# Kernel tuning notes

Measured on AMD Instinct MI355X. Metric: run time of the kernel, lower is better.

## Reference

```python
import jax, jax.numpy as jnp
import numpy as np

HIDDEN = 4096
NQ = 32        # query heads
NKV = 8        # kv heads
HD = 128       # head dim
EPS = 1e-6
BASE = 10000.0
T = 2048


def setup_inputs() -> dict:
    key = jax.random.key(0)
    ks = jax.random.split(key, 4)
    s = 0.02
    return {
        "hidden_states": jax.random.normal(ks[0], (T, HIDDEN), jnp.float32),
        "w_qkv": jax.random.normal(ks[1], ((NQ + 2 * NKV) * HD, HIDDEN), jnp.float32) * s,
        "q_norm_w": jnp.ones((HD,), jnp.float32),
        "k_norm_w": jnp.ones((HD,), jnp.float32),
        "w_o": jax.random.normal(ks[2], (HIDDEN, NQ * HD), jnp.float32) * s,
        "positions": jnp.arange(T, dtype=jnp.int64),
    }


def _rms_norm(x, w):
    # x: [T, H, D], normalize over last dim
    var = jnp.mean(jnp.square(x), axis=-1, keepdims=True)
    return x * jax.lax.rsqrt(var + EPS) * w


def _rope(x, positions):
    # neox-style: split halves. x: [T, H, D]
    half = HD // 2
    inv_freq = 1.0 / (BASE ** (jnp.arange(0, HD, 2, dtype=jnp.float32) / HD))  # [half]
    ang = positions.astype(jnp.float32)[:, None] * inv_freq  # [T, half]
    cos = jnp.cos(ang)[:, None, :]  # [T, 1, half]
    sin = jnp.sin(ang)[:, None, :]
    x1, x2 = x[..., :half], x[..., half:]
    return jnp.concatenate([x1 * cos - x2 * sin, x2 * cos + x1 * sin], axis=-1)


def reference(hidden_states, w_qkv, q_norm_w, k_norm_w, w_o, positions):
    t = hidden_states.shape[0]
    qkv = hidden_states @ w_qkv.T  # [T, (NQ+2*NKV)*HD]
    q, k, v = jnp.split(qkv, [NQ * HD, (NQ + NKV) * HD], axis=-1)
    q = _rms_norm(q.reshape(t, NQ, HD), q_norm_w)
    k = _rms_norm(k.reshape(t, NKV, HD), k_norm_w)
    v = v.reshape(t, NKV, HD)
    q = _rope(q, positions)
    k = _rope(k, positions)

    g = NQ // NKV
    qg = q.reshape(t, NKV, g, HD).transpose(1, 2, 0, 3)  # [NKV, g, T, HD]
    kt = k.transpose(1, 0, 2)  # [NKV, T, HD]
    vt = v.transpose(1, 0, 2)
    scale = HD ** -0.5
    scores = jnp.einsum('hgqd,hkd->hgqk', qg, kt) * scale  # [NKV, g, T, T]
    causal = positions[:, None] >= positions[None, :]  # [T, T]
    scores = jnp.where(causal[None, None], scores, jnp.float32(-1e30))
    p = jax.nn.softmax(scores, axis=-1)
    o = jnp.einsum('hgqk,hkd->hgqd', p, vt)  # [NKV, g, T, HD]
    o = o.transpose(2, 0, 1, 3).reshape(t, NQ * HD)
    return o @ w_o.T
```

## Files before the change

### kernel.cpp

```cpp
#include <hip/hip_runtime.h>
#include <hip/hip_bf16.h>

typedef float f32x4 __attribute__((ext_vector_type(4)));
typedef short s16x8 __attribute__((ext_vector_type(8)));
typedef short s16x4 __attribute__((ext_vector_type(4)));
typedef unsigned short u16;

#define HIDDEN 4096
#define NQ 32
#define NKV 8
#define HD 128
#define T_SEQ 2048
#define QKV_N ((NQ + 2 * NKV) * HD)

__device__ __forceinline__ u16 f2bf(float f) {
    union { float f; unsigned u; } v; v.f = f;
    unsigned r = v.u + 0x7FFFu + ((v.u >> 16) & 1u);
    return (u16)(r >> 16);
}
__device__ __forceinline__ float b2f(u16 h) {
    union { unsigned u; float f; } v; v.u = ((unsigned)h) << 16; return v.f;
}
__device__ __forceinline__ void gload_lds16(const u16* g, u16* l) {
    __builtin_amdgcn_global_load_lds(
        (const __attribute__((address_space(1))) unsigned int*)g,
        (__attribute__((address_space(3))) unsigned int*)l,
        16, 0, 0);
}
__device__ __forceinline__ int xcd_swz(int flat, int nwg) {
    return (flat & 7) * (nwg >> 3) + (flat >> 3);
}

__device__ __forceinline__ void conv8(const float* src, u16* dst, int i) {
    const float4 a = ((const float4*)src)[2 * i];
    const float4 b = ((const float4*)src)[2 * i + 1];
    s16x8 o;
    o[0] = (short)f2bf(a.x); o[1] = (short)f2bf(a.y);
    o[2] = (short)f2bf(a.z); o[3] = (short)f2bf(a.w);
    o[4] = (short)f2bf(b.x); o[5] = (short)f2bf(b.y);
    o[6] = (short)f2bf(b.z); o[7] = (short)f2bf(b.w);
    ((s16x8*)dst)[i] = o;
}
__global__ __launch_bounds__(256) void conv2_bf16_kern(
    const float* __restrict__ s1, u16* __restrict__ d1, int n1,
    const float* __restrict__ s2, u16* __restrict__ d2, int n2)
{
    for (int i = blockIdx.x * 256 + threadIdx.x; i < n1 + n2; i += gridDim.x * 256) {
        if (i < n1) conv8(s1, d1, i);
        else        conv8(s2, d2, i - n1);
    }
}

__global__ __launch_bounds__(512) void gemm1_4ph(
    const u16* __restrict__ A, const u16* __restrict__ B,
    u16* __restrict__ C, int N, int K)
{
    __shared__ u16 As[2][256 * 64];
    __shared__ u16 Bs[2][192 * 64];
    const int tid = threadIdx.x, lane = tid & 63, wid = tid >> 6;
    const int wr = wid >> 2, wc = wid & 3;
    const int lg = lane >> 4, l15 = lane & 15;
    const int m0 = blockIdx.y * 256, n0 = blockIdx.x * 192;
    const int nk = K >> 6;
    const int r8 = lane >> 3;
    const int csw = ((lane & 7) ^ r8) * 8;

    f32x4 acc[8][3] = {};
    s16x8 af[4][2], bq[3][2];

    auto stageA = [&](int sl, int c, int kt) {
        gload_lds16(&A[(size_t)(m0 + c * 64 + wid * 8 + r8) * K + kt * 64 + csw],
                    &As[sl][(c * 64 + wid * 8) * 64]);
    };
    auto stageB = [&](int sl, int c, int kt) {
        gload_lds16(&B[(size_t)(n0 + c * 64 + wid * 8 + r8) * K + kt * 64 + csw],
                    &Bs[sl][(c * 64 + wid * 8) * 64]);
    };
    auto ldA2 = [&](int s_, int mh_) {
#pragma unroll
        for (int mi = 0; mi < 4; ++mi)
#pragma unroll
            for (int kh = 0; kh < 2; ++kh)
                af[mi][kh] = *(const s16x8*)&As[s_][
                    ((wr * 128 + mh_ * 64 + mi * 16 + l15) << 6) +
                    (((lg + kh * 4) ^ (l15 & 7)) << 3)];
    };
    auto ldB2 = [&](int s_) {
#pragma unroll
        for (int ni = 0; ni < 3; ++ni)
#pragma unroll
            for (int kh = 0; kh < 2; ++kh)
                bq[ni][kh] = *(const s16x8*)&Bs[s_][
                    ((wc * 48 + ni * 16 + l15) << 6) +
                    (((lg + kh * 4) ^ (l15 & 7)) << 3)];
    };
    auto mm2 = [&](int mh_) {
        __builtin_amdgcn_s_setprio(1);
#pragma unroll
        for (int mi = 0; mi < 4; ++mi)
#pragma unroll
            for (int ni = 0; ni < 3; ++ni)
#pragma unroll
                for (int kh = 0; kh < 2; ++kh)
                    acc[mh_ * 4 + mi][ni] =
                        __builtin_amdgcn_mfma_f32_16x16x32_bf16(
                            af[mi][kh], bq[ni][kh], acc[mh_ * 4 + mi][ni], 0, 0, 0);
        __builtin_amdgcn_s_setprio(0);
    };
#define FENCE asm volatile("" ::: "memory");

    stageA(0, 0, 0); stageA(0, 1, 0); stageA(0, 2, 0); stageA(0, 3, 0);
    stageB(0, 0, 0); stageB(0, 1, 0); stageB(0, 2, 0);
    stageA(1, 0, 1); stageA(1, 2, 1);
    asm volatile("s_waitcnt vmcnt(2)" ::: "memory");
    __builtin_amdgcn_s_barrier();

    for (int t = 0; t < nk; ++t) {
        const int s = t & 1;
        ldA2(s, 0); ldB2(s);
        if (t + 1 < nk) {
            stageA(s ^ 1, 1, t + 1); stageA(s ^ 1, 3, t + 1);
            stageB(s ^ 1, 0, t + 1); stageB(s ^ 1, 1, t + 1); stageB(s ^ 1, 2, t + 1);
        }
        FENCE
        __builtin_amdgcn_s_barrier();
        mm2(0);
        FENCE
        __builtin_amdgcn_s_barrier();
        ldA2(s, 1);
        if (t + 2 < nk) { stageA(s, 0, t + 2); stageA(s, 2, t + 2); }
        FENCE
        __builtin_amdgcn_s_barrier();
        mm2(1);
        if (t + 2 < nk) asm volatile("s_waitcnt vmcnt(2)" ::: "memory");
        else            asm volatile("s_waitcnt vmcnt(0)" ::: "memory");
        FENCE
        __builtin_amdgcn_s_barrier();
    }

#pragma unroll
    for (int mh = 0; mh < 2; ++mh)
#pragma unroll
    for (int mi = 0; mi < 4; ++mi)
#pragma unroll
    for (int ni = 0; ni < 3; ++ni) {
        int row0 = m0 + wr * 128 + mh * 64 + mi * 16 + lg * 4;
        int col  = n0 + wc * 48 + ni * 16 + l15;
#pragma unroll
        for (int r = 0; r < 4; ++r)
            C[(size_t)(row0 + r) * N + col] = f2bf(acc[mh * 4 + mi][ni][r]);
    }
}

__global__ __launch_bounds__(512) void gemm2_2ph(
    const u16* __restrict__ A, const u16* __restrict__ B,
    float* __restrict__ C, int N, int K)
{
    __shared__ u16 As[3][256 * 64];
    __shared__ u16 Bs[3][128 * 64];
    const int tid = threadIdx.x, lane = tid & 63, wid = tid >> 6;
    const int wr = wid >> 2, wc = wid & 3;
    const int lg = lane >> 4, l15 = lane & 15;
    const int m0 = blockIdx.y * 256, n0 = blockIdx.x * 128;
    const int nk = K >> 6;
    const int r8 = lane >> 3;
    const int csw = ((lane & 7) ^ r8) * 8;

    f32x4 acc[8][2] = {};
    s16x8 af[8][2], bq[2][2];

    auto stageAll = [&](int sl, int kt) {
#pragma unroll
        for (int c = 0; c < 4; ++c)
            gload_lds16(&A[(size_t)(m0 + c * 64 + wid * 8 + r8) * K + kt * 64 + csw],
                        &As[sl][(c * 64 + wid * 8) * 64]);
#pragma unroll
        for (int c = 0; c < 2; ++c)
            gload_lds16(&B[(size_t)(n0 + c * 64 + wid * 8 + r8) * K + kt * 64 + csw],
                        &Bs[sl][(c * 64 + wid * 8) * 64]);
    };
    auto ldAll = [&](int s_) {
#pragma unroll
        for (int mi = 0; mi < 8; ++mi)
#pragma unroll
            for (int kh = 0; kh < 2; ++kh)
                af[mi][kh] = *(const s16x8*)&As[s_][
                    ((wr * 128 + mi * 16 + l15) << 6) +
                    (((lg + kh * 4) ^ (l15 & 7)) << 3)];
#pragma unroll
        for (int ni = 0; ni < 2; ++ni)
#pragma unroll
            for (int kh = 0; kh < 2; ++kh)
                bq[ni][kh] = *(const s16x8*)&Bs[s_][
                    ((wc * 32 + ni * 16 + l15) << 6) +
                    (((lg + kh * 4) ^ (l15 & 7)) << 3)];
    };
    auto mmAll = [&]() {
        __builtin_amdgcn_s_setprio(1);
#pragma unroll
        for (int mi = 0; mi < 8; ++mi)
#pragma unroll
            for (int ni = 0; ni < 2; ++ni)
#pragma unroll
                for (int kh = 0; kh < 2; ++kh)
                    acc[mi][ni] = __builtin_amdgcn_mfma_f32_16x16x32_bf16(
                        af[mi][kh], bq[ni][kh], acc[mi][ni], 0, 0, 0);
        __builtin_amdgcn_s_setprio(0);
    };
#define FENCE asm volatile("" ::: "memory");

    stageAll(0, 0);
    stageAll(1, 1);
    asm volatile("s_waitcnt vmcnt(6)" ::: "memory");
    __builtin_amdgcn_s_barrier();

    int s = 0;
    for (int t = 0; t < nk; ++t) {
        ldAll(s);
        if (t + 2 < nk) {
            int s2 = s + 2; if (s2 >= 3) s2 -= 3;
            stageAll(s2, t + 2);
        }
        FENCE
        __builtin_amdgcn_s_barrier();
        mmAll();
        if (t + 2 < nk) asm volatile("s_waitcnt vmcnt(6)" ::: "memory");
        else            asm volatile("s_waitcnt vmcnt(0)" ::: "memory");
        FENCE
        __builtin_amdgcn_s_barrier();
        if (++s >= 3) s -= 3;
    }
#undef FENCE

#pragma unroll
    for (int mi = 0; mi < 8; ++mi)
#pragma unroll
    for (int ni = 0; ni < 2; ++ni) {
        int row0 = m0 + wr * 128 + mi * 16 + lg * 4;
        int col  = n0 + wc * 32 + ni * 16 + l15;
#pragma unroll
        for (int r = 0; r < 4; ++r)
            C[(size_t)(row0 + r) * N + col] = acc[mi][ni][r];
    }
}

__global__ __launch_bounds__(256) void nr_vt_kern(
    const u16* __restrict__ qkv, const float* __restrict__ qw,
    const float* __restrict__ kw, u16* __restrict__ qr, u16* __restrict__ kr,
    u16* __restrict__ vt)
{
    __shared__ u16 Ts[128][66];
    const int id = blockIdx.x, tid = threadIdx.x;
    if (id < 20480) {
        const int t = id & 2047, h = (id >> 11) * 4 + (tid >> 6);
        const int i = tid & 63;
        const size_t rowbase = (size_t)t * QKV_N;
        const u16* src; const float* w; u16* dst;
        if (h < 32) {
            src = qkv + rowbase + h * HD; w = qw;
            dst = qr + ((size_t)h * T_SEQ + t) * HD;
        } else {
            int kh = h - 32;
            src = qkv + rowbase + NQ * HD + kh * HD; w = kw;
            dst = kr + ((size_t)kh * T_SEQ + t) * HD;
        }
        float x1 = b2f(src[i]), x2 = b2f(src[i + 64]);
        float ss = x1 * x1 + x2 * x2;
#pragma unroll
        for (int d = 32; d >= 1; d >>= 1) ss += __shfl_xor(ss, d);
        float rs = rsqrtf(ss * (1.0f / 128.0f) + 1e-6f);
        x1 *= rs * w[i];
        x2 *= rs * w[i + 64];
        float ang = (float)t * exp2f((float)i * -0.20762050593567985f);
        float sn, cs;
        sincosf(ang, &sn, &cs);
        dst[i]      = f2bf(x1 * cs - x2 * sn);
        dst[i + 64] = f2bf(x2 * cs + x1 * sn);
        return;
    }
    const int id2 = id - 20480;
    const int t0 = (id2 & 31) * 64, kh = id2 >> 5;
#pragma unroll
    for (int it = 0; it < 4; ++it) {
        int slot = tid + it * 256;
        int tl = slot >> 4, dc = (slot & 15) * 8;
        s16x8 v = *(const s16x8*)&qkv[(size_t)(t0 + tl) * QKV_N + (NQ + NKV) * HD + kh * HD + dc];
#pragma unroll
        for (int e = 0; e < 8; ++e) Ts[dc + e][tl] = (u16)v[e];
    }
    __syncthreads();
#pragma unroll
    for (int it = 0; it < 4; ++it) {
        int slot = tid + it * 256;
        int d = slot >> 3, c = (slot & 7) * 8;
        s16x8 v = *(const s16x8*)&Ts[d][c];
        *(s16x8*)&vt[((size_t)kh * HD + d) * T_SEQ + t0 + c] = v;
    }
}

#define KS(b, r, c) Ks[(b)][((r) << 7) + ((c) ^ (((r) & 7) << 3))]
#define VS(b, r, c) Vs[(b)][((r) << 6) + ((c) ^ (((r) & 7) << 3))]
#define PS(wv, r, c) Ps[((wv) << 10) + ((r) << 6) + ((c) ^ (((r) & 7) << 3))]

__global__ __launch_bounds__(512) void attn_kern(
    const u16* __restrict__ qr, const u16* __restrict__ kr,
    const u16* __restrict__ vt, u16* __restrict__ o,
    const float* __restrict__ wo, u16* __restrict__ wo_bf)
{
    __shared__ u16 Ks[2][64 * 128];
    __shared__ u16 Vs[2][128 * 64];
    __shared__ u16 Ps[8 * 16 * 64];
    const int tid = threadIdx.x, lane = tid & 63, w = tid >> 6;
    const int lg = lane >> 4, l15 = lane & 15;
    const int fb = (int)blockIdx.y * 8 + (int)blockIdx.x;
    const int flat = xcd_swz(fb, 256);
    const int qh = flat >> 3, bx = flat & 7;
    const int kvh = qh >> 2;
    const float scale2 = 0.08838834764831845f * 1.4426950408889634f;

    const int cvbase = fb * 8192 + tid;
    int cv = 0;
    float4 cva = {}, cvb = {};

    const int krow = tid >> 4, kcol = (tid & 15) * 8;
    const int vrow = tid >> 3, vcol = (tid & 7) * 8;
    const u16* krbase = kr + (size_t)kvh * T_SEQ * HD;
    const u16* vtbase = vt + (size_t)kvh * HD * T_SEQ;

    s16x8 kst[2], vst[2];
#define LOADKV(k0_) do { \
    kst[0] = *(const s16x8*)&krbase[(size_t)((k0_) + krow) * HD + kcol]; \
    kst[1] = *(const s16x8*)&krbase[(size_t)((k0_) + krow + 32) * HD + kcol]; \
    vst[0] = *(const s16x8*)&vtbase[(size_t)(vrow) * T_SEQ + (k0_) + vcol]; \
    vst[1] = *(const s16x8*)&vtbase[(size_t)(vrow + 64) * T_SEQ + (k0_) + vcol]; \
    } while (0)
#define WRITEKV(b) do { \
    *(s16x8*)&KS((b), krow, kcol) = kst[0]; \
    *(s16x8*)&KS((b), krow + 32, kcol) = kst[1]; \
    *(s16x8*)&VS((b), vrow, vcol) = vst[0]; \
    *(s16x8*)&VS((b), vrow + 64, vcol) = vst[1]; \
    } while (0)

    for (int half = 0; half < 2; ++half) {
        const int q0 = (half == 0) ? bx * 128 : (T_SEQ - 128) - bx * 128;
        s16x8 qf[4];
        {
            const u16* qb = qr + ((size_t)qh * T_SEQ + q0 + w * 16 + l15) * HD;
#pragma unroll
            for (int dc = 0; dc < 4; ++dc) qf[dc] = *(const s16x8*)&qb[dc * 32 + lg * 8];
        }
        f32x4 oacc[8] = {};
        float mQ = -1e30f, lsQ = 0.f;

        const int ktiles = (q0 >> 6) + 2;
        LOADKV(0);
        WRITEKV(0);
        __syncthreads();
        for (int kt = 0; kt < ktiles; ++kt) {
            const int k0 = kt * 64;
            const int cur = kt & 1;
            if (kt + 1 < ktiles) LOADKV(k0 + 64);

            if (cv <= 16) {
                if (cv > 0) {
                    s16x8 o8;
                    o8[0] = (short)f2bf(cva.x); o8[1] = (short)f2bf(cva.y);
                    o8[2] = (short)f2bf(cva.z); o8[3] = (short)f2bf(cva.w);
                    o8[4] = (short)f2bf(cvb.x); o8[5] = (short)f2bf(cvb.y);
                    o8[6] = (short)f2bf(cvb.z); o8[7] = (short)f2bf(cvb.w);
                    ((s16x8*)wo_bf)[cvbase + (cv - 1) * 512] = o8;
                }
                if (cv < 16) {
                    cva = ((const float4*)wo)[2 * (cvbase + cv * 512)];
                    cvb = ((const float4*)wo)[2 * (cvbase + cv * 512) + 1];
                }
                ++cv;
            }

            f32x4 sc[4] = {};
            __builtin_amdgcn_s_setprio(1);
#pragma unroll
            for (int nc = 0; nc < 4; ++nc)
#pragma unroll
                for (int dc = 0; dc < 4; ++dc) {
                    s16x8 kf = *(const s16x8*)&KS(cur, nc * 16 + l15, dc * 32 + lg * 8);
                    sc[nc] = __builtin_amdgcn_mfma_f32_16x16x32_bf16(kf, qf[dc], sc[nc], 0, 0, 0);
                }
            __builtin_amdgcn_s_setprio(0);

            const int qg = q0 + w * 16 + l15;
            const bool needMask = (k0 + 63) > (q0 + w * 16);
            float tm = -1e30f;
#pragma unroll
            for (int nc = 0; nc < 4; ++nc)
#pragma unroll
                for (int r = 0; r < 4; ++r) {
                    float v = sc[nc][r] * scale2;
                    int kg = k0 + nc * 16 + lg * 4 + r;
                    if (needMask && kg > qg) v = -1e30f;
                    sc[nc][r] = v;
                    tm = fmaxf(tm, v);
                }
            tm = fmaxf(tm, __shfl_xor(tm, 16));
            tm = fmaxf(tm, __shfl_xor(tm, 32));

            if (__any(tm > mQ + 8.0f)) {
                float mn = fmaxf(mQ, tm);
                float alpha = exp2f(mQ - mn);
                mQ = mn;
                lsQ *= alpha;
                float aq[4];
#pragma unroll
                for (int r = 0; r < 4; ++r) aq[r] = __shfl(alpha, lg * 4 + r);
#pragma unroll
                for (int dc = 0; dc < 8; ++dc)
#pragma unroll
                    for (int r = 0; r < 4; ++r) oacc[dc][r] *= aq[r];
            }

            float ts = 0.f;
#pragma unroll
            for (int nc = 0; nc < 4; ++nc) {
                s16x4 pk;
#pragma unroll
                for (int r = 0; r < 4; ++r) {
                    float e = exp2f(sc[nc][r] - mQ);
                    ts += e;
                    pk[r] = (short)f2bf(e);
                }
                *(s16x4*)&PS(w, l15, nc * 16 + lg * 4) = pk;
            }
            ts += __shfl_xor(ts, 16);
            ts += __shfl_xor(ts, 32);
            lsQ += ts;

            __builtin_amdgcn_s_setprio(1);
#pragma unroll
            for (int kc = 0; kc < 2; ++kc) {
                s16x8 pf = *(const s16x8*)&PS(w, l15, kc * 32 + lg * 8);
#pragma unroll
                for (int dc = 0; dc < 8; ++dc) {
                    s16x8 vf = *(const s16x8*)&VS(cur, dc * 16 + l15, kc * 32 + lg * 8);
                    oacc[dc] = __builtin_amdgcn_mfma_f32_16x16x32_bf16(pf, vf, oacc[dc], 0, 0, 0);
                }
            }
            __builtin_amdgcn_s_setprio(0);

            if (kt + 1 < ktiles) WRITEKV(cur ^ 1);
            __syncthreads();
        }
        float lq[4];
#pragma unroll
        for (int r = 0; r < 4; ++r) lq[r] = __shfl(lsQ, lg * 4 + r);
#pragma unroll
        for (int r = 0; r < 4; ++r) {
            float inv = 1.0f / lq[r];
            int trow = q0 + w * 16 + lg * 4 + r;
            u16* dst = o + (size_t)trow * (NQ * HD) + qh * HD;
#pragma unroll
            for (int dc = 0; dc < 8; ++dc) dst[dc * 16 + l15] = f2bf(oacc[dc][r] * inv);
        }
    }
#undef LOADKV
#undef WRITEKV
}

extern "C" void kernel_launch(void* const* d_in, const int* in_sizes, int n_in,
                              void* d_out, int out_size, void* d_ws, size_t ws_size,
                              hipStream_t stream)
{
    const float* hs   = (const float*)d_in[0];
    const float* wqkv = (const float*)d_in[1];
    const float* qw   = (const float*)d_in[2];
    const float* kw   = (const float*)d_in[3];
    const float* wo   = (const float*)d_in[4];
    float* out = (float*)d_out;

    char* ws = (char*)d_ws;
    u16* hs_bf   = (u16*)(ws);
    u16* ob      = (u16*)(ws);
    u16* qkv_bf  = (u16*)(ws + 16777216);
    u16* wo_bf   = (u16*)(ws + 16777216);
    u16* wqkv_bf = (u16*)(ws + 41943040);
    u16* qr      = (u16*)(ws + 67108864);
    u16* kr      = (u16*)(ws + 83886080);
    u16* vt      = (u16*)(ws + 88080384);

    conv2_bf16_kern<<<2048, 256, 0, stream>>>(
        hs, hs_bf, T_SEQ * HIDDEN / 8, wqkv, wqkv_bf, QKV_N * HIDDEN / 8);
    gemm1_4ph<<<dim3(QKV_N / 192, T_SEQ / 256), 512, 0, stream>>>(
        hs_bf, wqkv_bf, qkv_bf, QKV_N, HIDDEN);
    nr_vt_kern<<<20736, 256, 0, stream>>>(qkv_bf, qw, kw, qr, kr, vt);
    attn_kern<<<dim3(8, NQ), 512, 0, stream>>>(qr, kr, vt, ob, wo, wo_bf);
    gemm2_2ph<<<dim3(HIDDEN / 128, T_SEQ / 256), 512, 0, stream>>>(
        ob, wo_bf, out, HIDDEN, HIDDEN);
}
```

Measured before the change: 301.5 us.

## Restructure QKV GEMM to two-phase loop with triple-buffered A tiles

Replaces the four-phase per-k-step schedule of the QKV projection GEMM with a two-phase one. All A and B fragments are loaded from LDS at once, then all MFMAs run. A tiles get a third LDS buffer so the next-next A tile can be prefetched while B is double-buffered. The aim is to halve barriers per k-step and give longer uninterrupted MFMA runs. The cost is more registers (8x2 A fragments held at once) and more LDS (an extra 32KB buffer), which could lower occupancy or cause spills.

Result: no change. 299.4 us (-0.7%).

```diff
diff --git a/kernel.cpp b/kernel.cpp
--- a/kernel.cpp
+++ b/kernel.cpp
@@ -51,11 +51,11 @@
     }
 }
 
-__global__ __launch_bounds__(512) void gemm1_4ph(
+__global__ __launch_bounds__(512) void gemm1_2ph(
     const u16* __restrict__ A, const u16* __restrict__ B,
     u16* __restrict__ C, int N, int K)
 {
-    __shared__ u16 As[2][256 * 64];
+    __shared__ u16 As[3][256 * 64];
     __shared__ u16 Bs[2][192 * 64];
     const int tid = threadIdx.x, lane = tid & 63, wid = tid >> 6;
     const int wr = wid >> 2, wc = wid & 3;
@@ -66,89 +66,85 @@
     const int csw = ((lane & 7) ^ r8) * 8;
 
     f32x4 acc[8][3] = {};
-    s16x8 af[4][2], bq[3][2];
-
-    auto stageA = [&](int sl, int c, int kt) {
-        gload_lds16(&A[(size_t)(m0 + c * 64 + wid * 8 + r8) * K + kt * 64 + csw],
-                    &As[sl][(c * 64 + wid * 8) * 64]);
-    };
-    auto stageB = [&](int sl, int c, int kt) {
-        gload_lds16(&B[(size_t)(n0 + c * 64 + wid * 8 + r8) * K + kt * 64 + csw],
-                    &Bs[sl][(c * 64 + wid * 8) * 64]);
-    };
-    auto ldA2 = [&](int s_, int mh_) {
-#pragma unroll
-        for (int mi = 0; mi < 4; ++mi)
+    s16x8 af[8][2], bq[3][2];
+
+    auto stageA = [&](int sl, int kt) {
+#pragma unroll
+        for (int c = 0; c < 4; ++c)
+            gload_lds16(&A[(size_t)(m0 + c * 64 + wid * 8 + r8) * K + kt * 64 + csw],
+                        &As[sl][(c * 64 + wid * 8) * 64]);
+    };
+    auto stageB = [&](int sl, int kt) {
+#pragma unroll
+        for (int c = 0; c < 3; ++c)
+            gload_lds16(&B[(size_t)(n0 + c * 64 + wid * 8 + r8) * K + kt * 64 + csw],
+                        &Bs[sl][(c * 64 + wid * 8) * 64]);
+    };
+    auto ldAll = [&](int s3_, int s2_) {
+#pragma unroll
+        for (int mi = 0; mi < 8; ++mi)
 #pragma unroll
             for (int kh = 0; kh < 2; ++kh)
-                af[mi][kh] = *(const s16x8*)&As[s_][
-                    ((wr * 128 + mh_ * 64 + mi * 16 + l15) << 6) +
+                af[mi][kh] = *(const s16x8*)&As[s3_][
+                    ((wr * 128 + mi * 16 + l15) << 6) +
                     (((lg + kh * 4) ^ (l15 & 7)) << 3)];
-    };
-    auto ldB2 = [&](int s_) {
 #pragma unroll
         for (int ni = 0; ni < 3; ++ni)
 #pragma unroll
             for (int kh = 0; kh < 2; ++kh)
-                bq[ni][kh] = *(const s16x8*)&Bs[s_][
+                bq[ni][kh] = *(const s16x8*)&Bs[s2_][
                     ((wc * 48 + ni * 16 + l15) << 6) +
                     (((lg + kh * 4) ^ (l15 & 7)) << 3)];
     };
-    auto mm2 = [&](int mh_) {
+    auto mmAll = [&]() {
         __builtin_amdgcn_s_setprio(1);
 #pragma unroll
-        for (int mi = 0; mi < 4; ++mi)
+        for (int mi = 0; mi < 8; ++mi)
 #pragma unroll
             for (int ni = 0; ni < 3; ++ni)
 #pragma unroll
                 for (int kh = 0; kh < 2; ++kh)
-                    acc[mh_ * 4 + mi][ni] =
-                        __builtin_amdgcn_mfma_f32_16x16x32_bf16(
-                            af[mi][kh], bq[ni][kh], acc[mh_ * 4 + mi][ni], 0, 0, 0);
+                    acc[mi][ni] = __builtin_amdgcn_mfma_f32_16x16x32_bf16(
+                        af[mi][kh], bq[ni][kh], acc[mi][ni], 0, 0, 0);
         __builtin_amdgcn_s_setprio(0);
     };
 #define FENCE asm volatile("" ::: "memory");
 
-    stageA(0, 0, 0); stageA(0, 1, 0); stageA(0, 2, 0); stageA(0, 3, 0);
-    stageB(0, 0, 0); stageB(0, 1, 0); stageB(0, 2, 0);
-    stageA(1, 0, 1); stageA(1, 2, 1);
-    asm volatile("s_waitcnt vmcnt(2)" ::: "memory");
+    stageA(0, 0);
+    stageB(0, 0);
+    stageA(1, 1);
+    asm volatile("s_waitcnt vmcnt(4)" ::: "memory");
     __builtin_amdgcn_s_barrier();
 
+    int s3 = 0;
     for (int t = 0; t < nk; ++t) {
-        const int s = t & 1;
-        ldA2(s, 0); ldB2(s);
-        if (t + 1 < nk) {
-            stageA(s ^ 1, 1, t + 1); stageA(s ^ 1, 3, t + 1);
-            stageB(s ^ 1, 0, t + 1); stageB(s ^ 1, 1, t + 1); stageB(s ^ 1, 2, t + 1);
+        const int s2 = t & 1;
+        ldAll(s3, s2);
+        if (t + 1 < nk) stageB(s2 ^ 1, t + 1);
+        if (t + 2 < nk) {
+            int sn = s3 + 2; if (sn >= 3) sn -= 3;
+            stageA(sn, t + 2);
         }
         FENCE
         __builtin_amdgcn_s_barrier();
-        mm2(0);
-        FENCE
-        __builtin_amdgcn_s_barrier();
-        ldA2(s, 1);
-        if (t + 2 < nk) { stageA(s, 0, t + 2); stageA(s, 2, t + 2); }
-        FENCE
-        __builtin_amdgcn_s_barrier();
-        mm2(1);
-        if (t + 2 < nk) asm volatile("s_waitcnt vmcnt(2)" ::: "memory");
+        mmAll();
+        if (t + 2 < nk) asm volatile("s_waitcnt vmcnt(4)" ::: "memory");
         else            asm volatile("s_waitcnt vmcnt(0)" ::: "memory");
         FENCE
         __builtin_amdgcn_s_barrier();
-    }
-
-#pragma unroll
-    for (int mh = 0; mh < 2; ++mh)
-#pragma unroll
-    for (int mi = 0; mi < 4; ++mi)
+        if (++s3 >= 3) s3 -= 3;
+    }
+#undef FENCE
+
+#pragma unroll
+    for (int mi = 0; mi < 8; ++mi)
 #pragma unroll
     for (int ni = 0; ni < 3; ++ni) {
-        int row0 = m0 + wr * 128 + mh * 64 + mi * 16 + lg * 4;
+        int row0 = m0 + wr * 128 + mi * 16 + lg * 4;
         int col  = n0 + wc * 48 + ni * 16 + l15;
 #pragma unroll
         for (int r = 0; r < 4; ++r)
-            C[(size_t)(row0 + r) * N + col] = f2bf(acc[mh * 4 + mi][ni][r]);
+            C[(size_t)(row0 + r) * N + col] = f2bf(acc[mi][ni][r]);
     }
 }
 
@@ -488,7 +484,7 @@
 
     conv2_bf16_kern<<<2048, 256, 0, stream>>>(
         hs, hs_bf, T_SEQ * HIDDEN / 8, wqkv, wqkv_bf, QKV_N * HIDDEN / 8);
-    gemm1_4ph<<<dim3(QKV_N / 192, T_SEQ / 256), 512, 0, stream>>>(
+    gemm1_2ph<<<dim3(QKV_N / 192, T_SEQ / 256), 512, 0, stream>>>(
         hs_bf, wqkv_bf, qkv_bf, QKV_N, HIDDEN);
     nr_vt_kern<<<20736, 256, 0, stream>>>(qkv_bf, qw, kw, qr, kr, vt);
     attn_kern<<<dim3(8, NQ), 512, 0, stream>>>(qr, kr, vt, ob, wo, wo_bf);
```
